# Optimization experiments

Measured on AMD Instinct MI355X. Metric: run time of the kernel, lower is better.

## Reference

```python
import jax, jax.numpy as jnp
import numpy as np

B, C, H, W = 4, 64, 64, 64
DQ = 64            # query/key dim (hardcoded 64 in the module)
FP_DIM = 128       # fingerprint_dim
SCALE = 1.0 / 8.0  # 1/sqrt(64)


def setup_inputs() -> dict:
    key = jax.random.key(0)
    ks = jax.random.split(key, 12)
    s = 0.05
    return {
        "x": jax.random.normal(ks[0], (B, C, H, W), jnp.float32),
        "fingerprint": jax.random.normal(ks[1], (B, FP_DIM), jnp.float32),
        # 1x1 conv weights stored as [out_ch, in_ch]
        "Wq": jax.random.normal(ks[2], (DQ, C), jnp.float32) * s,
        "bq": jax.random.normal(ks[3], (DQ,), jnp.float32) * s,
        "Wk": jax.random.normal(ks[4], (DQ, C), jnp.float32) * s,
        "bk": jax.random.normal(ks[5], (DQ,), jnp.float32) * s,
        "Wv": jax.random.normal(ks[6], (C, C), jnp.float32) * s,
        "bv": jax.random.normal(ks[7], (C,), jnp.float32) * s,
        "Wo": jax.random.normal(ks[8], (C, C), jnp.float32) * s,
        "bo": jax.random.normal(ks[9], (C,), jnp.float32) * s,
        "Wfp": jax.random.normal(ks[10], (DQ, FP_DIM), jnp.float32) * s,
        "bfp": jax.random.normal(ks[11], (DQ,), jnp.float32) * s,
    }


def reference(x, fingerprint, Wq, bq, Wk, bk, Wv, bv, Wo, bo, Wfp, bfp):
    b, c, h, w = x.shape
    # fingerprint projection: Linear(fingerprint_dim, 64)
    fp_proj = fingerprint @ Wfp.T + bfp                      # [B, 64]
    # 1x1 convs as channel einsums
    q = jnp.einsum('bchw,oc->bohw', x, Wq) + bq[None, :, None, None]  # [B,64,H,W]
    k = jnp.einsum('bchw,oc->bohw', x, Wk) + bk[None, :, None, None]  # [B,64,H,W]
    v = jnp.einsum('bchw,oc->bohw', x, Wv) + bv[None, :, None, None]  # [B,C,H,W]
    qf = q.reshape(b, DQ, h * w)   # [B,64,N]
    kf = k.reshape(b, DQ, h * w)   # [B,64,N]
    vf = v.reshape(b, c, h * w)    # [B,C,N]
    # attn[b,i,j] = <q_i, k_j>/sqrt(64), softmax over keys j
    attn = jax.nn.softmax(jnp.einsum('bdi,bdj->bij', qf, kf) * SCALE, axis=2)  # [B,N,N]
    out = jnp.einsum('bcj,bij->bci', vf, attn).reshape(b, c, h, w)
    # fingerprint-gated modulation map
    attn_map = jax.nn.sigmoid(jnp.einsum('bdhw,bd->bhw', q, fp_proj))[:, None]  # [B,1,H,W]
    out = out * attn_map + x
    out = jnp.einsum('bchw,oc->bohw', out, Wo) + bo[None, :, None, None]
    return out
```

## Files before the change

kernel.cpp:

```cpp
#include <hip/hip_runtime.h>
#include <cstdint>
#include <cstddef>

#define B_    4
#define C_    64
#define N_    4096
#define FPD_  128
#define QSCALE_ (0.125f * 1.4426950408889634f)

#if __has_builtin(__builtin_amdgcn_exp2f)
#define EXP2(x) __builtin_amdgcn_exp2f(x)
#else
#define EXP2(x) exp2f(x)
#endif

typedef short bf16x8 __attribute__((ext_vector_type(8)));
typedef float f32x4  __attribute__((ext_vector_type(4)));

__device__ inline unsigned short f2bf(float f) {
    union { float f; unsigned int u; } v; v.f = f;
    unsigned int u = v.u;
    return (unsigned short)((u + 0x7FFFu + ((u >> 16) & 1u)) >> 16);
}
__device__ inline unsigned int pack2bf(float a, float b) {
    return (unsigned int)f2bf(a) | ((unsigned int)f2bf(b) << 16);
}
__device__ inline unsigned short f2bf_fast(float f) {
    union { float f; unsigned int u; } v; v.f = f;
    return (unsigned short)((v.u + 0x8000u) >> 16);
}
__device__ inline float bflo(unsigned int u) {
    union { unsigned int u; float f; } v; v.u = u << 16; return v.f;
}
__device__ inline float bfhi(unsigned int u) {
    union { unsigned int u; float f; } v; v.u = u & 0xFFFF0000u; return v.f;
}

__global__ __launch_bounds__(256) void qkv_kernel(
    const float* __restrict__ x,
    const float* __restrict__ Wq, const float* __restrict__ bq,
    const float* __restrict__ Wk, const float* __restrict__ bk,
    const float* __restrict__ Wv, const float* __restrict__ bv,
    const float* __restrict__ fp, const float* __restrict__ Wfp,
    const float* __restrict__ bfp,
    float* __restrict__ gate,
    unsigned short* __restrict__ Qb, unsigned short* __restrict__ Kb,
    unsigned short* __restrict__ Vb)
{
    __shared__ unsigned short xT[64 * 72];
    __shared__ unsigned short Wl[64 * 72];
    __shared__ unsigned short rp[64 * 72];
    __shared__ float gredf[256];
    __shared__ float fpp[64];

    int tid  = threadIdx.x;
    int bx   = blockIdx.x;
    int pass = bx >> 8;
    int rem  = bx & 255;
    int b  = rem >> 6;
    int p0 = (rem & 63) << 6;
    const float* xb = x + (size_t)b * (C_ * N_) + p0;

    const float* Wsrc = (pass == 0) ? Wq : (pass == 1) ? Wk : Wv;
    const float* bsrc = (pass == 0) ? bq : (pass == 1) ? bk : bv;
    float wscale = (pass == 0) ? QSCALE_ : 1.0f;

    {
        int o  = tid >> 2;
        int cb = (tid & 3) << 4;
        const float4* src = reinterpret_cast<const float4*>(&Wsrc[o * 64 + cb]);
        float4 w0 = src[0], w1 = src[1], w2 = src[2], w3 = src[3];
        uint4 lo, hi;
        lo.x = pack2bf(w0.x * wscale, w0.y * wscale);
        lo.y = pack2bf(w0.z * wscale, w0.w * wscale);
        lo.z = pack2bf(w1.x * wscale, w1.y * wscale);
        lo.w = pack2bf(w1.z * wscale, w1.w * wscale);
        hi.x = pack2bf(w2.x * wscale, w2.y * wscale);
        hi.y = pack2bf(w2.z * wscale, w2.w * wscale);
        hi.z = pack2bf(w3.x * wscale, w3.y * wscale);
        hi.w = pack2bf(w3.z * wscale, w3.w * wscale);
        *reinterpret_cast<uint4*>(&Wl[o * 72 + cb])     = lo;
        *reinterpret_cast<uint4*>(&Wl[o * 72 + cb + 8]) = hi;
    }
    #pragma unroll
    for (int i = 0; i < 4; ++i) {
        int u = tid + i * 256;
        int c = u >> 4, p4 = (u & 15) << 2;
        float4 v = *reinterpret_cast<const float4*>(&xb[(size_t)c * N_ + p4]);
        xT[(p4 + 0) * 72 + c] = f2bf(v.x);
        xT[(p4 + 1) * 72 + c] = f2bf(v.y);
        xT[(p4 + 2) * 72 + c] = f2bf(v.z);
        xT[(p4 + 3) * 72 + c] = f2bf(v.w);
    }
    if (pass == 0) {
        int d = tid >> 2, kq = tid & 3;
        const float4* wrow = reinterpret_cast<const float4*>(&Wfp[d * FPD_ + kq * 32]);
        const float4* frow = reinterpret_cast<const float4*>(&fp[b * FPD_ + kq * 32]);
        float s = 0.f;
        #pragma unroll
        for (int i = 0; i < 8; ++i) {
            float4 w4 = wrow[i], f4 = frow[i];
            s += w4.x * f4.x + w4.y * f4.y + w4.z * f4.z + w4.w * f4.w;
        }
        gredf[tid] = s;
    }
    __syncthreads();
    if (pass == 0 && tid < 64)
        fpp[tid] = bfp[tid] + gredf[tid * 4] + gredf[tid * 4 + 1]
                 + gredf[tid * 4 + 2] + gredf[tid * 4 + 3];
    if (pass == 0) __syncthreads();

    int lane = tid & 63;
    int wv   = __builtin_amdgcn_readfirstlane(tid >> 6);
    int quad = lane >> 4, l16 = lane & 15;
    int prow = wv * 16 + l16;

    bf16x8 bx0 = *reinterpret_cast<bf16x8*>(&xT[prow * 72 + quad * 8]);
    bf16x8 bx1 = *reinterpret_cast<bf16x8*>(&xT[prow * 72 + 32 + quad * 8]);

    float gp = 0.f;
    #pragma unroll
    for (int t4 = 0; t4 < 4; ++t4) {
        bf16x8 a0 = *reinterpret_cast<bf16x8*>(&Wl[(t4 * 16 + l16) * 72 + quad * 8]);
        bf16x8 a1 = *reinterpret_cast<bf16x8*>(&Wl[(t4 * 16 + l16) * 72 + 32 + quad * 8]);
        f32x4 c4 = (f32x4){0.f, 0.f, 0.f, 0.f};
        c4 = __builtin_amdgcn_mfma_f32_16x16x32_bf16(a0, bx0, c4, 0, 0, 0);
        c4 = __builtin_amdgcn_mfma_f32_16x16x32_bf16(a1, bx1, c4, 0, 0, 0);
        float4 bias = *reinterpret_cast<const float4*>(&bsrc[t4 * 16 + quad * 4]);
        c4[0] += bias.x * wscale; c4[1] += bias.y * wscale;
        c4[2] += bias.z * wscale; c4[3] += bias.w * wscale;
        if (pass == 0) {
            gp = fmaf(c4[0], fpp[t4 * 16 + quad * 4 + 0], gp);
            gp = fmaf(c4[1], fpp[t4 * 16 + quad * 4 + 1], gp);
            gp = fmaf(c4[2], fpp[t4 * 16 + quad * 4 + 2], gp);
            gp = fmaf(c4[3], fpp[t4 * 16 + quad * 4 + 3], gp);
        }
        if (pass < 2) {
            int dd = t4 * 16 + quad * 4;
            *reinterpret_cast<ushort2*>(&rp[prow * 72 + dd]) =
                (ushort2){f2bf(c4[0]), f2bf(c4[1])};
            *reinterpret_cast<ushort2*>(&rp[prow * 72 + dd + 2]) =
                (ushort2){f2bf(c4[2]), f2bf(c4[3])};
        } else {
            #pragma unroll
            for (int j = 0; j < 4; ++j)
                rp[(t4 * 16 + quad * 4 + j) * 72 + prow] = f2bf(c4[j]);
        }
    }
    if (pass == 0) {
        gp += __shfl_xor(gp, 16);
        gp += __shfl_xor(gp, 32);
        if (lane < 16) {
            int pos = p0 + wv * 16 + lane;
            float s = gp * (1.0f / QSCALE_);
            gate[b * N_ + pos] = 1.f / (1.f + __expf(-s));
        }
    }
    __syncthreads();

    int row = tid >> 2;
    int cb  = (tid & 3) << 4;
    ushort4 u[4];
    #pragma unroll
    for (int k = 0; k < 4; ++k)
        u[k] = *reinterpret_cast<ushort4*>(&rp[row * 72 + cb + k * 4]);
    unsigned short* dst;
    if (pass == 0)      dst = Qb + ((size_t)b * N_ + p0 + row) * 64 + cb;
    else if (pass == 1) dst = Kb + ((size_t)b * N_ + p0 + row) * 64 + cb;
    else                dst = Vb + ((size_t)b * 64 + row) * N_ + p0 + cb;
    #pragma unroll
    for (int k = 0; k < 4; ++k)
        *reinterpret_cast<ushort4*>(dst + k * 4) = u[k];
}

__global__ __launch_bounds__(256, 2) void attn_kernel(
    const unsigned short* __restrict__ Qb, const unsigned short* __restrict__ Kb,
    const unsigned short* __restrict__ Vb, unsigned short* __restrict__ Opart,
    float* __restrict__ lpart)
{
    __shared__ unsigned short Ks[64 * 72];
    __shared__ unsigned short Vs[64 * 72];
    __shared__ unsigned short Ps[128 * 72];

    int tid = threadIdx.x;
    int bx  = blockIdx.x;
    int qt  = bx >> 4;
    int grp = bx & 15;
    int b   = grp >> 2;
    int ks  = grp & 3;
    int q0  = qt << 7;
    int kbase = ks << 10;

    int lane = tid & 63;
    int wv   = __builtin_amdgcn_readfirstlane(tid >> 6);
    int quad = lane >> 4, l16 = lane & 15;
    int qs0  = wv << 5;

    const unsigned short* Qg = Qb + ((size_t)b * N_ + q0) * 64;
    bf16x8 aq[2][2];
    #pragma unroll
    for (int s = 0; s < 2; ++s) {
        aq[s][0] = *reinterpret_cast<const bf16x8*>(
            &Qg[(qs0 + s * 16 + l16) * 64 + quad * 8]);
        aq[s][1] = *reinterpret_cast<const bf16x8*>(
            &Qg[(qs0 + s * 16 + l16) * 64 + 32 + quad * 8]);
    }

    const unsigned short* Kg = Kb + ((size_t)b * N_ + kbase) * 64;
    const unsigned short* Vg = Vb + (size_t)b * 64 * N_ + kbase;

    int r0 = tid >> 4;
    int cc = (tid & 15) << 2;

    ushort4 kr[4], vr[4];
    #pragma unroll
    for (int i = 0; i < 4; ++i) {
        int r = r0 + 16 * i;
        kr[i] = *reinterpret_cast<const ushort4*>(&Kg[(size_t)r * 64 + cc]);
        vr[i] = *reinterpret_cast<const ushort4*>(&Vg[(size_t)r * N_ + cc]);
    }

    f32x4 oacc[2][4]; f32x4 lacc[2];
    #pragma unroll
    for (int s = 0; s < 2; ++s) {
        lacc[s] = (f32x4){0.f, 0.f, 0.f, 0.f};
        #pragma unroll
        for (int cs = 0; cs < 4; ++cs) oacc[s][cs] = (f32x4){0.f, 0.f, 0.f, 0.f};
    }
    bf16x8 ones;
    #pragma unroll
    for (int i = 0; i < 8; ++i) ones[i] = (short)0x3F80;

    for (int kt = 0; kt < 16; ++kt) {
        __syncthreads();
        #pragma unroll
        for (int i = 0; i < 4; ++i) {
            int r = r0 + 16 * i;
            *reinterpret_cast<ushort4*>(&Ks[r * 72 + cc]) = kr[i];
            *reinterpret_cast<ushort4*>(&Vs[r * 72 + cc]) = vr[i];
        }
        __syncthreads();
        if (kt < 15) {
            int kk = (kt + 1) << 6;
            #pragma unroll
            for (int i = 0; i < 4; ++i) {
                int r = r0 + 16 * i;
                kr[i] = *reinterpret_cast<const ushort4*>(&Kg[(size_t)(kk + r) * 64 + cc]);
                vr[i] = *reinterpret_cast<const ushort4*>(&Vg[(size_t)r * N_ + kk + cc]);
            }
        }

        #pragma unroll
        for (int kj = 0; kj < 4; ++kj) {
            bf16x8 bk0 = *reinterpret_cast<bf16x8*>(&Ks[(kj * 16 + l16) * 72 + quad * 8]);
            bf16x8 bk1 = *reinterpret_cast<bf16x8*>(&Ks[(kj * 16 + l16) * 72 + 32 + quad * 8]);
            #pragma unroll
            for (int s = 0; s < 2; ++s) {
                f32x4 sv = (f32x4){0.f, 0.f, 0.f, 0.f};
                sv = __builtin_amdgcn_mfma_f32_16x16x32_bf16(aq[s][0], bk0, sv, 0, 0, 0);
                sv = __builtin_amdgcn_mfma_f32_16x16x32_bf16(aq[s][1], bk1, sv, 0, 0, 0);
                #pragma unroll
                for (int j = 0; j < 4; ++j) {
                    float pv = EXP2(sv[j]);
                    Ps[(qs0 + s * 16 + quad * 4 + j) * 72 + kj * 16 + l16] = f2bf_fast(pv);
                }
            }
        }
        __asm__ volatile("s_waitcnt lgkmcnt(0)" ::: "memory");

        bf16x8 ap[2][2];
        #pragma unroll
        for (int s = 0; s < 2; ++s) {
            ap[s][0] = *reinterpret_cast<bf16x8*>(&Ps[(qs0 + s * 16 + l16) * 72 + quad * 8]);
            ap[s][1] = *reinterpret_cast<bf16x8*>(&Ps[(qs0 + s * 16 + l16) * 72 + 32 + quad * 8]);
            lacc[s] = __builtin_amdgcn_mfma_f32_16x16x32_bf16(ap[s][0], ones, lacc[s], 0, 0, 0);
            lacc[s] = __builtin_amdgcn_mfma_f32_16x16x32_bf16(ap[s][1], ones, lacc[s], 0, 0, 0);
        }
        #pragma unroll
        for (int cs = 0; cs < 4; ++cs) {
            bf16x8 bv0 = *reinterpret_cast<bf16x8*>(&Vs[(cs * 16 + l16) * 72 + quad * 8]);
            bf16x8 bv1 = *reinterpret_cast<bf16x8*>(&Vs[(cs * 16 + l16) * 72 + 32 + quad * 8]);
            #pragma unroll
            for (int s = 0; s < 2; ++s) {
                oacc[s][cs] = __builtin_amdgcn_mfma_f32_16x16x32_bf16(ap[s][0], bv0, oacc[s][cs], 0, 0, 0);
                oacc[s][cs] = __builtin_amdgcn_mfma_f32_16x16x32_bf16(ap[s][1], bv1, oacc[s][cs], 0, 0, 0);
            }
        }
    }

    unsigned short* Og = Opart + (((size_t)ks * B_ + b) * N_ + q0) * 64;
    #pragma unroll
    for (int s = 0; s < 2; ++s)
        #pragma unroll
        for (int j = 0; j < 4; ++j) {
            int row = qs0 + s * 16 + quad * 4 + j;
            #pragma unroll
            for (int cs = 0; cs < 4; ++cs)
                Og[row * 64 + cs * 16 + l16] = f2bf_fast(oacc[s][cs][j]);
        }
    if (l16 == 0) {
        #pragma unroll
        for (int s = 0; s < 2; ++s)
            #pragma unroll
            for (int j = 0; j < 4; ++j)
                lpart[((size_t)ks * B_ + b) * N_ + q0 + qs0 + s * 16 + quad * 4 + j]
                    = lacc[s][j];
    }
}

__global__ __launch_bounds__(256) void epi_kernel(
    const unsigned short* __restrict__ Opart, const float* __restrict__ lpart,
    const float* __restrict__ x, const float* __restrict__ gate,
    const float* __restrict__ Wo, const float* __restrict__ bo,
    float* __restrict__ out)
{
    __shared__ float xs[64 * 68];
    __shared__ float osum[64 * 68];
    __shared__ unsigned short Wl[32 * 72];
    __shared__ float os[32 * 68];

    int tid  = threadIdx.x;
    int bx   = blockIdx.x;
    int half = bx >> 8;
    int rem  = bx & 255;
    int b  = rem >> 6;
    int p0 = (rem & 63) << 6;
    const float* xb = x + (size_t)b * (C_ * N_) + p0;

    #pragma unroll
    for (int i = 0; i < 4; ++i) {
        int u = tid + i * 256;
        int c = u >> 4, p4 = (u & 15) << 2;
        float4 v = *reinterpret_cast<const float4*>(&xb[(size_t)c * N_ + p4]);
        xs[(p4 + 0) * 68 + c] = v.x;
        xs[(p4 + 1) * 68 + c] = v.y;
        xs[(p4 + 2) * 68 + c] = v.z;
        xs[(p4 + 3) * 68 + c] = v.w;
    }
    {
        const unsigned short* Ob = Opart + ((size_t)b * N_ + p0) * 64;
        const size_t kstride = (size_t)B_ * N_ * 64;
        #pragma unroll
        for (int i = 0; i < 4; ++i) {
            int u = tid + i * 256;
            int p = u >> 4, c4 = (u & 15) << 2;
            size_t off = (size_t)p * 64 + c4;
            uint2 a0 = *reinterpret_cast<const uint2*>(&Ob[off]);
            uint2 a1 = *reinterpret_cast<const uint2*>(&Ob[off + kstride]);
            uint2 a2 = *reinterpret_cast<const uint2*>(&Ob[off + 2 * kstride]);
            uint2 a3 = *reinterpret_cast<const uint2*>(&Ob[off + 3 * kstride]);
            float4 ssum;
            ssum.x = (bflo(a0.x) + bflo(a1.x)) + (bflo(a2.x) + bflo(a3.x));
            ssum.y = (bfhi(a0.x) + bfhi(a1.x)) + (bfhi(a2.x) + bfhi(a3.x));
            ssum.z = (bflo(a0.y) + bflo(a1.y)) + (bflo(a2.y) + bflo(a3.y));
            ssum.w = (bfhi(a0.y) + bfhi(a1.y)) + (bfhi(a2.y) + bfhi(a3.y));
            *reinterpret_cast<float4*>(&osum[p * 68 + c4]) = ssum;
        }
    }
    {
        int ol = tid >> 3;
        int cb = (tid & 7) << 3;
        const float4* src = reinterpret_cast<const float4*>(
            &Wo[(half * 32 + ol) * 64 + cb]);
        float4 w0 = src[0], w1 = src[1];
        uint2 pkd;
        pkd.x = pack2bf(w0.x, w0.y); pkd.y = pack2bf(w0.z, w0.w);
        *reinterpret_cast<uint2*>(&Wl[ol * 72 + cb]) = pkd;
        pkd.x = pack2bf(w1.x, w1.y); pkd.y = pack2bf(w1.z, w1.w);
        *reinterpret_cast<uint2*>(&Wl[ol * 72 + cb + 4]) = pkd;
    }
    __syncthreads();

    int lane = tid & 63;
    int wv   = __builtin_amdgcn_readfirstlane(tid >> 6);
    int quad = lane >> 4, l16 = lane & 15;
    int prow = wv * 16 + l16;
    int pos  = p0 + prow;

    float lv = lpart[(size_t)b * N_ + pos]
             + lpart[((size_t)B_ + b) * N_ + pos]
             + lpart[(2 * (size_t)B_ + b) * N_ + pos]
             + lpart[(3 * (size_t)B_ + b) * N_ + pos];
    float gi = gate[b * N_ + pos] / lv;

    bf16x8 bt[2];
    #pragma unroll
    for (int chunk = 0; chunk < 2; ++chunk) {
        int cb2 = chunk * 32 + quad * 8;
        float4 oa = *reinterpret_cast<float4*>(&osum[prow * 68 + cb2]);
        float4 ob4 = *reinterpret_cast<float4*>(&osum[prow * 68 + cb2 + 4]);
        float4 xa = *reinterpret_cast<float4*>(&xs[prow * 68 + cb2]);
        float4 xb4 = *reinterpret_cast<float4*>(&xs[prow * 68 + cb2 + 4]);
        bt[chunk][0] = f2bf(fmaf(oa.x, gi, xa.x));
        bt[chunk][1] = f2bf(fmaf(oa.y, gi, xa.y));
        bt[chunk][2] = f2bf(fmaf(oa.z, gi, xa.z));
        bt[chunk][3] = f2bf(fmaf(oa.w, gi, xa.w));
        bt[chunk][4] = f2bf(fmaf(ob4.x, gi, xb4.x));
        bt[chunk][5] = f2bf(fmaf(ob4.y, gi, xb4.y));
        bt[chunk][6] = f2bf(fmaf(ob4.z, gi, xb4.z));
        bt[chunk][7] = f2bf(fmaf(ob4.w, gi, xb4.w));
    }

    #pragma unroll
    for (int tt = 0; tt < 2; ++tt) {
        int ot = half * 2 + tt;
        bf16x8 a0 = *reinterpret_cast<bf16x8*>(&Wl[(tt * 16 + l16) * 72 + quad * 8]);
        bf16x8 a1 = *reinterpret_cast<bf16x8*>(&Wl[(tt * 16 + l16) * 72 + 32 + quad * 8]);
        f32x4 c4 = (f32x4){0.f, 0.f, 0.f, 0.f};
        c4 = __builtin_amdgcn_mfma_f32_16x16x32_bf16(a0, bt[0], c4, 0, 0, 0);
        c4 = __builtin_amdgcn_mfma_f32_16x16x32_bf16(a1, bt[1], c4, 0, 0, 0);
        float4 bias = *reinterpret_cast<const float4*>(&bo[ot * 16 + quad * 4]);
        c4[0] += bias.x; c4[1] += bias.y; c4[2] += bias.z; c4[3] += bias.w;
        #pragma unroll
        for (int j = 0; j < 4; ++j)
            os[(tt * 16 + quad * 4 + j) * 68 + prow] = c4[j];
    }
    __syncthreads();

    int row = tid >> 3;
    int pb  = (tid & 7) << 3;
    float* ob = out + ((size_t)b * 64 + half * 32 + row) * N_ + p0 + pb;
    *reinterpret_cast<float4*>(ob)     = *reinterpret_cast<float4*>(&os[row * 68 + pb]);
    *reinterpret_cast<float4*>(ob + 4) = *reinterpret_cast<float4*>(&os[row * 68 + pb + 4]);
}

extern "C" void kernel_launch(void* const* d_in, const int* in_sizes, int n_in,
                              void* d_out, int out_size, void* d_ws, size_t ws_size,
                              hipStream_t stream)
{
    const float* x   = (const float*)d_in[0];
    const float* fp  = (const float*)d_in[1];
    const float* Wq  = (const float*)d_in[2];
    const float* bq  = (const float*)d_in[3];
    const float* Wk  = (const float*)d_in[4];
    const float* bk  = (const float*)d_in[5];
    const float* Wv  = (const float*)d_in[6];
    const float* bv  = (const float*)d_in[7];
    const float* Wo  = (const float*)d_in[8];
    const float* bo  = (const float*)d_in[9];
    const float* Wfp = (const float*)d_in[10];
    const float* bfp = (const float*)d_in[11];
    float* out = (float*)d_out;

    char* ws = (char*)d_ws;
    float* gate = (float*)(ws);
    unsigned short* Qb = (unsigned short*)(ws + 65536);
    unsigned short* Kb = (unsigned short*)(ws + 65536 + 2097152);
    unsigned short* Vb = (unsigned short*)(ws + 65536 + 2 * 2097152);
    unsigned short* Opart = (unsigned short*)(ws + 65536 + 3 * 2097152);
    float* lpart = (float*)(ws + 65536 + 3 * 2097152 + 8388608);


    hipLaunchKernelGGL(qkv_kernel, dim3(768), dim3(256), 0, stream,
                       x, Wq, bq, Wk, bk, Wv, bv, fp, Wfp, bfp,
                       gate, Qb, Kb, Vb);
    hipLaunchKernelGGL(attn_kernel, dim3(512), dim3(256), 0, stream,
                       Qb, Kb, Vb, Opart, lpart);
    hipLaunchKernelGGL(epi_kernel, dim3(512), dim3(256), 0, stream,
                       Opart, lpart, x, gate, Wo, bo, out);
}
```

Baseline: 118.6 us.

## Swap QK MFMA operands, load K directly, compute row sums in registers, merge epilogue halves

The attention kernel swaps the QK^T MFMA operands so K fragments are read straight from global memory, which removes the K shared-memory tile and its staging. P is now written transposed as packed bf16 pairs. Row sums are accumulated in fp32 registers with cross-lane shuffles instead of extra MFMAs against a ones vector. V staging uses wider 16-byte loads. The epilogue kernel now computes all 64 output channels per block instead of splitting them across two blocks, which halves the grid and avoids redundant x/osum loading, at the cost of more shared memory per block and lower parallelism.

```diff
diff --git a/kernel.cpp b/kernel.cpp
--- a/kernel.cpp
+++ b/kernel.cpp
@@ -28,6 +28,10 @@
 __device__ inline unsigned short f2bf_fast(float f) {
     union { float f; unsigned int u; } v; v.f = f;
     return (unsigned short)((v.u + 0x8000u) >> 16);
+}
+__device__ inline unsigned int pack2bf_fast(float a, float b) {
+    union { float f; unsigned int u; } ua, ub; ua.f = a; ub.f = b;
+    return ((ua.u + 0x8000u) >> 16) | ((ub.u + 0x8000u) & 0xFFFF0000u);
 }
 __device__ inline float bflo(unsigned int u) {
     union { unsigned int u; float f; } v; v.u = u << 16; return v.f;
@@ -178,7 +182,6 @@
     const unsigned short* __restrict__ Vb, unsigned short* __restrict__ Opart,
     float* __restrict__ lpart)
 {
-    __shared__ unsigned short Ks[64 * 72];
     __shared__ unsigned short Vs[64 * 72];
     __shared__ unsigned short Ps[128 * 72];
 
@@ -197,74 +200,79 @@
     int qs0  = wv << 5;
 
     const unsigned short* Qg = Qb + ((size_t)b * N_ + q0) * 64;
-    bf16x8 aq[2][2];
+    bf16x8 bq[2][2];
     #pragma unroll
     for (int s = 0; s < 2; ++s) {
-        aq[s][0] = *reinterpret_cast<const bf16x8*>(
+        bq[s][0] = *reinterpret_cast<const bf16x8*>(
             &Qg[(qs0 + s * 16 + l16) * 64 + quad * 8]);
-        aq[s][1] = *reinterpret_cast<const bf16x8*>(
+        bq[s][1] = *reinterpret_cast<const bf16x8*>(
             &Qg[(qs0 + s * 16 + l16) * 64 + 32 + quad * 8]);
     }
 
     const unsigned short* Kg = Kb + ((size_t)b * N_ + kbase) * 64;
     const unsigned short* Vg = Vb + (size_t)b * 64 * N_ + kbase;
 
-    int r0 = tid >> 4;
-    int cc = (tid & 15) << 2;
-
-    ushort4 kr[4], vr[4];
-    #pragma unroll
-    for (int i = 0; i < 4; ++i) {
-        int r = r0 + 16 * i;
-        kr[i] = *reinterpret_cast<const ushort4*>(&Kg[(size_t)r * 64 + cc]);
-        vr[i] = *reinterpret_cast<const ushort4*>(&Vg[(size_t)r * N_ + cc]);
-    }
-
-    f32x4 oacc[2][4]; f32x4 lacc[2];
-    #pragma unroll
-    for (int s = 0; s < 2; ++s) {
-        lacc[s] = (f32x4){0.f, 0.f, 0.f, 0.f};
+    int srow = tid >> 3;
+    int scol = (tid & 7) << 3;
+
+    uint4 vr[2];
+    #pragma unroll
+    for (int i = 0; i < 2; ++i) {
+        int r = srow + 32 * i;
+        vr[i] = *reinterpret_cast<const uint4*>(&Vg[(size_t)r * N_ + scol]);
+    }
+
+    f32x4 oacc[2][4]; float lacc[2] = {0.f, 0.f};
+    #pragma unroll
+    for (int s = 0; s < 2; ++s)
         #pragma unroll
         for (int cs = 0; cs < 4; ++cs) oacc[s][cs] = (f32x4){0.f, 0.f, 0.f, 0.f};
-    }
-    bf16x8 ones;
-    #pragma unroll
-    for (int i = 0; i < 8; ++i) ones[i] = (short)0x3F80;
 
     for (int kt = 0; kt < 16; ++kt) {
+        int k0 = kt << 6;
         __syncthreads();
         #pragma unroll
-        for (int i = 0; i < 4; ++i) {
-            int r = r0 + 16 * i;
-            *reinterpret_cast<ushort4*>(&Ks[r * 72 + cc]) = kr[i];
-            *reinterpret_cast<ushort4*>(&Vs[r * 72 + cc]) = vr[i];
+        for (int i = 0; i < 2; ++i) {
+            int r = srow + 32 * i;
+            *reinterpret_cast<uint4*>(&Vs[r * 72 + scol]) = vr[i];
         }
         __syncthreads();
         if (kt < 15) {
             int kk = (kt + 1) << 6;
             #pragma unroll
-            for (int i = 0; i < 4; ++i) {
-                int r = r0 + 16 * i;
-                kr[i] = *reinterpret_cast<const ushort4*>(&Kg[(size_t)(kk + r) * 64 + cc]);
-                vr[i] = *reinterpret_cast<const ushort4*>(&Vg[(size_t)r * N_ + kk + cc]);
+            for (int i = 0; i < 2; ++i) {
+                int r = srow + 32 * i;
+                vr[i] = *reinterpret_cast<const uint4*>(&Vg[(size_t)r * N_ + kk + scol]);
             }
         }
 
+        float ls[2] = {0.f, 0.f};
         #pragma unroll
         for (int kj = 0; kj < 4; ++kj) {
-            bf16x8 bk0 = *reinterpret_cast<bf16x8*>(&Ks[(kj * 16 + l16) * 72 + quad * 8]);
-            bf16x8 bk1 = *reinterpret_cast<bf16x8*>(&Ks[(kj * 16 + l16) * 72 + 32 + quad * 8]);
+            const unsigned short* Kr = &Kg[(size_t)(k0 + kj * 16 + l16) * 64 + quad * 8];
+            bf16x8 ak0 = *reinterpret_cast<const bf16x8*>(Kr);
+            bf16x8 ak1 = *reinterpret_cast<const bf16x8*>(Kr + 32);
             #pragma unroll
             for (int s = 0; s < 2; ++s) {
                 f32x4 sv = (f32x4){0.f, 0.f, 0.f, 0.f};
-                sv = __builtin_amdgcn_mfma_f32_16x16x32_bf16(aq[s][0], bk0, sv, 0, 0, 0);
-                sv = __builtin_amdgcn_mfma_f32_16x16x32_bf16(aq[s][1], bk1, sv, 0, 0, 0);
-                #pragma unroll
-                for (int j = 0; j < 4; ++j) {
-                    float pv = EXP2(sv[j]);
-                    Ps[(qs0 + s * 16 + quad * 4 + j) * 72 + kj * 16 + l16] = f2bf_fast(pv);
-                }
+                sv = __builtin_amdgcn_mfma_f32_16x16x32_bf16(ak0, bq[s][0], sv, 0, 0, 0);
+                sv = __builtin_amdgcn_mfma_f32_16x16x32_bf16(ak1, bq[s][1], sv, 0, 0, 0);
+                float p0v = EXP2(sv[0]), p1v = EXP2(sv[1]);
+                float p2v = EXP2(sv[2]), p3v = EXP2(sv[3]);
+                ls[s] += (p0v + p1v) + (p2v + p3v);
+                uint2 pk;
+                pk.x = pack2bf_fast(p0v, p1v);
+                pk.y = pack2bf_fast(p2v, p3v);
+                *reinterpret_cast<uint2*>(
+                    &Ps[(qs0 + s * 16 + l16) * 72 + kj * 16 + quad * 4]) = pk;
             }
+        }
+        #pragma unroll
+        for (int s = 0; s < 2; ++s) {
+            float v = ls[s];
+            v += __shfl_xor(v, 16);
+            v += __shfl_xor(v, 32);
+            lacc[s] += v;
         }
         __asm__ volatile("s_waitcnt lgkmcnt(0)" ::: "memory");
 
@@ -273,8 +281,6 @@
         for (int s = 0; s < 2; ++s) {
             ap[s][0] = *reinterpret_cast<bf16x8*>(&Ps[(qs0 + s * 16 + l16) * 72 + quad * 8]);
             ap[s][1] = *reinterpret_cast<bf16x8*>(&Ps[(qs0 + s * 16 + l16) * 72 + 32 + quad * 8]);
-            lacc[s] = __builtin_amdgcn_mfma_f32_16x16x32_bf16(ap[s][0], ones, lacc[s], 0, 0, 0);
-            lacc[s] = __builtin_amdgcn_mfma_f32_16x16x32_bf16(ap[s][1], ones, lacc[s], 0, 0, 0);
         }
         #pragma unroll
         for (int cs = 0; cs < 4; ++cs) {
@@ -298,13 +304,10 @@
             for (int cs = 0; cs < 4; ++cs)
                 Og[row * 64 + cs * 16 + l16] = f2bf_fast(oacc[s][cs][j]);
         }
-    if (l16 == 0) {
+    if (quad == 0) {
         #pragma unroll
         for (int s = 0; s < 2; ++s)
-            #pragma unroll
-            for (int j = 0; j < 4; ++j)
-                lpart[((size_t)ks * B_ + b) * N_ + q0 + qs0 + s * 16 + quad * 4 + j]
-                    = lacc[s][j];
+            lpart[((size_t)ks * B_ + b) * N_ + q0 + qs0 + s * 16 + l16] = lacc[s];
     }
 }
 
@@ -316,15 +319,13 @@
 {
     __shared__ float xs[64 * 68];
     __shared__ float osum[64 * 68];
-    __shared__ unsigned short Wl[32 * 72];
-    __shared__ float os[32 * 68];
+    __shared__ unsigned short Wl[64 * 72];
+    __shared__ float os[64 * 68];
 
     int tid  = threadIdx.x;
     int bx   = blockIdx.x;
-    int half = bx >> 8;
-    int rem  = bx & 255;
-    int b  = rem >> 6;
-    int p0 = (rem & 63) << 6;
+    int b  = bx >> 6;
+    int p0 = (bx & 63) << 6;
     const float* xb = x + (size_t)b * (C_ * N_) + p0;
 
     #pragma unroll
@@ -358,16 +359,17 @@
         }
     }
     {
-        int ol = tid >> 3;
-        int cb = (tid & 7) << 3;
-        const float4* src = reinterpret_cast<const float4*>(
-            &Wo[(half * 32 + ol) * 64 + cb]);
-        float4 w0 = src[0], w1 = src[1];
-        uint2 pkd;
-        pkd.x = pack2bf(w0.x, w0.y); pkd.y = pack2bf(w0.z, w0.w);
-        *reinterpret_cast<uint2*>(&Wl[ol * 72 + cb]) = pkd;
-        pkd.x = pack2bf(w1.x, w1.y); pkd.y = pack2bf(w1.z, w1.w);
-        *reinterpret_cast<uint2*>(&Wl[ol * 72 + cb + 4]) = pkd;
+        int ol = tid >> 2;
+        int cb = (tid & 3) << 4;
+        const float4* src = reinterpret_cast<const float4*>(&Wo[ol * 64 + cb]);
+        float4 w0 = src[0], w1 = src[1], w2 = src[2], w3 = src[3];
+        uint4 lo, hi;
+        lo.x = pack2bf(w0.x, w0.y); lo.y = pack2bf(w0.z, w0.w);
+        lo.z = pack2bf(w1.x, w1.y); lo.w = pack2bf(w1.z, w1.w);
+        hi.x = pack2bf(w2.x, w2.y); hi.y = pack2bf(w2.z, w2.w);
+        hi.z = pack2bf(w3.x, w3.y); hi.w = pack2bf(w3.z, w3.w);
+        *reinterpret_cast<uint4*>(&Wl[ol * 72 + cb])     = lo;
+        *reinterpret_cast<uint4*>(&Wl[ol * 72 + cb + 8]) = hi;
     }
     __syncthreads();
 
@@ -402,14 +404,13 @@
     }
 
     #pragma unroll
-    for (int tt = 0; tt < 2; ++tt) {
-        int ot = half * 2 + tt;
+    for (int tt = 0; tt < 4; ++tt) {
         bf16x8 a0 = *reinterpret_cast<bf16x8*>(&Wl[(tt * 16 + l16) * 72 + quad * 8]);
         bf16x8 a1 = *reinterpret_cast<bf16x8*>(&Wl[(tt * 16 + l16) * 72 + 32 + quad * 8]);
         f32x4 c4 = (f32x4){0.f, 0.f, 0.f, 0.f};
         c4 = __builtin_amdgcn_mfma_f32_16x16x32_bf16(a0, bt[0], c4, 0, 0, 0);
         c4 = __builtin_amdgcn_mfma_f32_16x16x32_bf16(a1, bt[1], c4, 0, 0, 0);
-        float4 bias = *reinterpret_cast<const float4*>(&bo[ot * 16 + quad * 4]);
+        float4 bias = *reinterpret_cast<const float4*>(&bo[tt * 16 + quad * 4]);
         c4[0] += bias.x; c4[1] += bias.y; c4[2] += bias.z; c4[3] += bias.w;
         #pragma unroll
         for (int j = 0; j < 4; ++j)
@@ -417,11 +418,13 @@
     }
     __syncthreads();
 
-    int row = tid >> 3;
-    int pb  = (tid & 7) << 3;
-    float* ob = out + ((size_t)b * 64 + half * 32 + row) * N_ + p0 + pb;
-    *reinterpret_cast<float4*>(ob)     = *reinterpret_cast<float4*>(&os[row * 68 + pb]);
-    *reinterpret_cast<float4*>(ob + 4) = *reinterpret_cast<float4*>(&os[row * 68 + pb + 4]);
+    int row = tid >> 2;
+    int pb  = (tid & 3) << 4;
+    float* ob = out + ((size_t)b * 64 + row) * N_ + p0 + pb;
+    #pragma unroll
+    for (int k = 0; k < 4; ++k)
+        *reinterpret_cast<float4*>(ob + k * 4) =
+            *reinterpret_cast<float4*>(&os[row * 68 + pb + k * 4]);
 }
 
 extern "C" void kernel_launch(void* const* d_in, const int* in_sizes, int n_in,
@@ -456,6 +459,6 @@
                        gate, Qb, Kb, Vb);
     hipLaunchKernelGGL(attn_kernel, dim3(512), dim3(256), 0, stream,
                        Qb, Kb, Vb, Opart, lpart);
-    hipLaunchKernelGGL(epi_kernel, dim3(512), dim3(256), 0, stream,
+    hipLaunchKernelGGL(epi_kernel, dim3(256), dim3(256), 0, stream,
                        Opart, lpart, x, gate, Wo, bo, out);
 }
```

Measured after the change: 145.5 us. 22.7% more time.
